# Optimization experiments

Hardware: AMD Instinct MI355X
Metric: run time of the kernel (lower is better)

Reference implementation:

```python
import jax, jax.numpy as jnp
import numpy as np

D_IN, E, K = 128, 256, 16
LN_EPS = 1e-5


def _layernorm(h, g, b):
    mu = jnp.mean(h, axis=-1, keepdims=True)
    var = jnp.mean(jnp.square(h - mu), axis=-1, keepdims=True)
    return (h - mu) * jax.lax.rsqrt(var + LN_EPS) * g + b


def _gelu(h):
    return jax.nn.gelu(h, approximate=False)  # torch F.gelu default = exact erf


def setup_inputs() -> dict:
    key = jax.random.key(0)
    ks = jax.random.split(key, 8)
    B, N = 8, 2048
    def lin(k, fan_in, fan_out):
        bound = 1.0 / np.sqrt(fan_in)
        return jax.random.uniform(k, (fan_in, fan_out), jnp.float32, -bound, bound)
    return {
        "x": jax.random.normal(ks[0], (B, N, D_IN), jnp.float32),
        "coordinates": jax.random.normal(ks[1], (B, N, 3), jnp.float32),
        "W1": lin(ks[2], 2 * D_IN, E), "b1": jnp.zeros((E,), jnp.float32),
        "g1": jnp.ones((E,), jnp.float32), "be1": jnp.zeros((E,), jnp.float32),
        "W2": lin(ks[3], E, E), "b2": jnp.zeros((E,), jnp.float32),
        "g2": jnp.ones((E,), jnp.float32), "be2": jnp.zeros((E,), jnp.float32),
        "W3": lin(ks[4], E, E), "b3": jnp.zeros((E,), jnp.float32),
        "g3": jnp.ones((E,), jnp.float32), "be3": jnp.zeros((E,), jnp.float32),
        "Ws": lin(ks[5], D_IN, E), "bs": jnp.zeros((E,), jnp.float32),
    }


def reference(x, coordinates, W1, b1, g1, be1, W2, b2, g2, be2, W3, b3, g3, be3, Ws, bs):
    B, N, D = x.shape
    # --- dynamic kNN graph: squared euclidean distances (sqrt is monotone, skip it) ---
    sq = jnp.sum(coordinates * coordinates, axis=-1)                 # [B,N]
    d2 = sq[:, :, None] + sq[:, None, :] - 2.0 * jnp.einsum(
        'bnc,bmc->bnm', coordinates, coordinates)                    # [B,N,N]
    d2 = jnp.maximum(d2, 0.0)
    _, idx = jax.lax.top_k(-d2, K)                                   # [B,N,K] nearest (incl. self)
    # --- gather neighbor features: neighbors[b,n,j] = x[b, idx[b,n,j]] ---
    neighbors = jax.vmap(lambda xb, ib: xb[ib])(x, idx)              # [B,N,K,D]
    central = jnp.broadcast_to(x[:, :, None, :], (B, N, K, D))       # [B,N,K,D]
    edge = jnp.concatenate([central, neighbors - central], axis=-1)  # [B,N,K,2D]
    # --- edge MLP: (Linear -> LN -> GELU) x3 ---
    h = _gelu(_layernorm(edge @ W1 + b1, g1, be1))
    h = _gelu(_layernorm(h @ W2 + b2, g2, be2))
    h = _gelu(_layernorm(h @ W3 + b3, g3, be3))                      # [B,N,K,E]
    # --- max aggregate over neighbors + shortcut ---
    agg = jnp.max(h, axis=2)                                         # [B,N,E]
    return _gelu(agg + x @ Ws + bs)
```

## Files before the change

### kernel.cpp

```cpp
#include <hip/hip_runtime.h>
#include <hip/hip_bf16.h>
#include <math.h>

#define B_ 8
#define N_ 2048
#define D_ 128
#define E_ 256
#define K_ 16
#define LN_EPS 1e-5f

typedef short bf16x8 __attribute__((ext_vector_type(8)));
typedef float f32x4 __attribute__((ext_vector_type(4)));
typedef float f32x2 __attribute__((ext_vector_type(2)));

__device__ __forceinline__ float sq3_ref(float x, float y, float z) {
#pragma clang fp contract(off)
    float s = x * x + y * y;
    s = s + z * z;
    return s;
}
__device__ __forceinline__ float d2_ref(float qx, float qy, float qz, float sqq,
                                        float mx, float my, float mz, float sqm) {
#pragma clang fp contract(off)
    float dot = mx * qx + my * qy;
    dot = dot + mz * qz;
    float t1 = sqq + sqm;
    float t2 = 2.0f * dot;
    float d2 = t1 - t2;
    return d2 > 0.0f ? d2 : 0.0f;
}

__device__ __forceinline__ unsigned pack2(float a, float b) {
    union { __hip_bfloat162 h2; unsigned u; } cv;
    cv.h2 = __float22bfloat162_rn(float2{a, b});
    return cv.u;
}

__device__ __forceinline__ f32x2 gelu2(f32x2 v) {
    const f32x2 w = v * v;
    f32x2 inner = w * 0.044715f;
    inner.x += 1.0f; inner.y += 1.0f;
    const f32x2 ue = (v * -2.3022083f) * inner;
    f32x2 t;
    t.x = __builtin_amdgcn_exp2f(ue.x);
    t.y = __builtin_amdgcn_exp2f(ue.y);
    f32x2 den = t;
    den.x += 1.0f; den.y += 1.0f;
    f32x2 r;
    r.x = __builtin_amdgcn_rcpf(den.x);
    r.y = __builtin_amdgcn_rcpf(den.y);
    return v * r;
}

__device__ __forceinline__ float dpp_rowmax16(float v) {
    int x = __float_as_int(v);
    v = fmaxf(v, __int_as_float(__builtin_amdgcn_mov_dpp(x, 0xB1, 0xF, 0xF, true)));
    x = __float_as_int(v);
    v = fmaxf(v, __int_as_float(__builtin_amdgcn_mov_dpp(x, 0x4E, 0xF, 0xF, true)));
    x = __float_as_int(v);
    v = fmaxf(v, __int_as_float(__builtin_amdgcn_mov_dpp(x, 0x141, 0xF, 0xF, true)));
    x = __float_as_int(v);
    v = fmaxf(v, __int_as_float(__builtin_amdgcn_mov_dpp(x, 0x140, 0xF, 0xF, true)));
    return v;
}

__global__ __launch_bounds__(512) void knn_select_kernel(const float* __restrict__ coords,
                                                         int* __restrict__ knn_out) {
    __shared__ float lc[3][N_];
    __shared__ float lsq[N_];
    __shared__ int cnt[8];
    const int wave = threadIdx.x >> 6;
    const int lane = threadIdx.x & 63;
    const int p = blockIdx.x * 8 + wave;
    const int b = p >> 11;
    const int n0 = p & (N_ - 1);
    const float* cb = coords + (size_t)b * N_ * 3;
    for (int i = threadIdx.x; i < N_ * 3; i += 512) {
        int n = i / 3, c = i - 3 * n;
        lc[c][n] = cb[i];
    }
    __syncthreads();
    for (int n = threadIdx.x; n < N_; n += 512) lsq[n] = sq3_ref(lc[0][n], lc[1][n], lc[2][n]);
    __syncthreads();

    const float qx = lc[0][n0], qy = lc[1][n0], qz = lc[2][n0], sqq = lsq[n0];
    unsigned key[32];
#pragma unroll
    for (int j = 0; j < 32; ++j) {
        const int m = j * 64 + lane;
        key[j] = __float_as_uint(d2_ref(qx, qy, qz, sqq, lc[0][m], lc[1][m], lc[2][m], lsq[m]));
    }

    unsigned prefix = 0;
    int rem = K_, setc = N_, bshift = 0;
    bool bounded = false;
    for (int bit = 31; bit >= 0; --bit) {
        const unsigned want = prefix << 1;
        int c = 0;
#pragma unroll
        for (int j = 0; j < 32; ++j) c += ((key[j] >> bit) == want) ? 1 : 0;
        for (int off = 1; off < 64; off <<= 1) c += __shfl_xor(c, off, 64);
        if (rem <= c) { prefix = want; setc = c; }
        else          { prefix = want | 1u; rem -= c; setc -= c; }
        bshift = bit;
        if (setc == rem) { bounded = true; break; }
    }

    if (lane == 0) cnt[wave] = 0;
    int* op = knn_out + (size_t)p * K_;
    const unsigned long long BE = bounded ? (((unsigned long long)prefix + 1ull) << bshift)
                                          : (unsigned long long)prefix;
#pragma unroll
    for (int j = 0; j < 32; ++j) {
        if ((unsigned long long)key[j] < BE) {
            int s = atomicAdd(&cnt[wave], 1);
            op[s] = j * 64 + lane;
        }
    }
    if (!bounded) {
        const unsigned V = prefix;
#pragma unroll
        for (int j = 0; j < 32; ++j) {
            if (rem > 0) {
                unsigned long long mask = __ballot(key[j] == V);
                int below = __popcll(mask & ((1ull << lane) - 1ull));
                if (key[j] == V && below < rem) {
                    int s = atomicAdd(&cnt[wave], 1);
                    op[s] = j * 64 + lane;
                }
                rem -= __popcll(mask);
            }
        }
    }
}

__global__ __launch_bounds__(64) void wprep_kernel(const float* __restrict__ W1,
                                                   const float* __restrict__ W2,
                                                   const float* __restrict__ W3,
                                                   const float* __restrict__ Ws,
                                                   short* __restrict__ WF) {
    const int bi = blockIdx.x;
    const int lane = threadIdx.x;
    const int g = lane >> 4, e = lane & 15;
    const float* W;
    int mt, kt;
    if (bi < 384) {
        const int L = bi >> 7;
        const int t = bi & 127;
        kt = t >> 4; mt = t & 15;
        W = (L == 0) ? W1 : (L == 1) ? W2 : W3;
    } else {
        const int t = bi - 384;
        kt = t >> 4; mt = t & 15;
        W = Ws;
    }
    const int f = 16 * mt + e;
    unsigned v[4];
#pragma unroll
    for (int i2 = 0; i2 < 4; ++i2) {
        const int k = 32 * kt + 8 * g + 2 * i2;
        v[i2] = pack2(W[(size_t)k * E_ + f], W[(size_t)(k + 1) * E_ + f]);
    }
    uint4 u; u.x = v[0]; u.y = v[1]; u.z = v[2]; u.w = v[3];
    *reinterpret_cast<uint4*>(WF + ((size_t)bi * 64 + lane) * 8) = u;
}

#define WCHUNKS 28

__device__ __forceinline__ void stage_chunk(const short* __restrict__ WF,
                                            short* __restrict__ dst,
                                            int c, int wave, int lane) {
    const short* src = WF + ((size_t)(c << 4) << 9);
#pragma unroll
    for (int i = 0; i < 4; ++i) {
        const int slot = (i << 8) + (wave << 6);
        const short* gp = src + ((size_t)(slot + lane) << 3);
        short* lp = dst + ((size_t)slot << 3);
        __builtin_amdgcn_global_load_lds(
            (const __attribute__((address_space(1))) void*)gp,
            (__attribute__((address_space(3))) void*)lp, 16, 0, 0);
    }
}

__global__ __launch_bounds__(256, 2) void edgeconv_mfma(
    const float* __restrict__ x, const int* __restrict__ knn,
    const short* __restrict__ WF,
    const float* __restrict__ b1, const float* __restrict__ g1, const float* __restrict__ be1,
    const float* __restrict__ b2, const float* __restrict__ g2, const float* __restrict__ be2,
    const float* __restrict__ b3, const float* __restrict__ g3, const float* __restrict__ be3,
    const float* __restrict__ bs,
    float* __restrict__ out)
{
    __shared__ short Hl[2][2][4096];
    __shared__ short Wbuf[2][8192];
    __shared__ short Hx[2][2][128];
    __shared__ float4 Xch[2][2][16];
    __shared__ float Pl[9 * 256];
    const int tid  = threadIdx.x;
    const int wave = tid >> 6;
    const int lane = tid & 63;
    const int wq = wave & 1;
    const int pr = wave >> 1;
    const int e = lane & 15;
    const int g = lane >> 4;
    const int p = blockIdx.x * 4 + wave;
    const int b = p >> 11;
    const int n = p & (N_ - 1);
    const unsigned swz = (unsigned)((e & 7) << 4);
    char* Hown = (char*)&Hl[pr][wq][0];
    char* Hp0  = (char*)&Hl[pr][0][0];
    char* Hp1  = (char*)&Hl[pr][1][0];
    char* XCo  = (char*)&Hx[pr][wq][0];
    const char* XC0 = (const char*)&Hx[pr][0][0];
    const char* XC1 = (const char*)&Hx[pr][1][0];

    stage_chunk(WF, &Wbuf[0][0], 0, wave, lane);

    {
        const float* srcs[9] = {b1, g1, be1, b2, g2, be2, b3, g3, be3};
#pragma unroll
        for (int a = 0; a < 9; ++a) Pl[a * 256 + tid] = srcs[a][tid];
    }

    {
        const float4* xr = (const float4*)(x + ((size_t)b * N_ + n) * D_);
        const int nb = knn[(size_t)p * K_ + e];
        const float4* nr = (const float4*)(x + ((size_t)b * N_ + nb) * D_);
#pragma unroll
        for (int c2 = 0; c2 < 8; ++c2) {
            const float4 cv = xr[8 * g + c2];
            const float4 nv = nr[8 * g + c2];
            const int base = (e << 9) + (g << 6) + (c2 << 3);
            const uint2 cpk = make_uint2(pack2(cv.x, cv.y), pack2(cv.z, cv.w));
            *(uint2*)(Hown + (base ^ swz)) = cpk;
            *(uint2*)(Hown + ((base + 256) ^ swz)) =
                make_uint2(pack2(nv.x - cv.x, nv.y - cv.y), pack2(nv.z - cv.z, nv.w - cv.w));
            if (e == 0) *(uint2*)(XCo + (g << 6) + (c2 << 3)) = cpk;
        }
    }

    f32x4 acc0[8], acc1[8];
    int pb = 0;
    const f32x4 z4 = {0.f, 0.f, 0.f, 0.f};

    for (int L = 0; L < 3; ++L) {
        const float* PlL = &Pl[L * 768];
#pragma unroll
        for (int mtl = 0; mtl < 8; ++mtl) { acc0[mtl] = z4; acc1[mtl] = z4; }

        for (int kt = 0; kt < 8; ++kt) {
            const int c = L * 8 + kt;
            asm volatile("s_waitcnt vmcnt(0)" ::: "memory");
            __syncthreads();
            if (c + 1 < WCHUNKS) stage_chunk(WF, &Wbuf[pb ^ 1][0], c + 1, wave, lane);
            const int offB = (int)((unsigned)((e << 9) + (kt << 6) + (g << 4)) ^ swz);
            const bf16x8 Bc0 = *(const bf16x8*)(Hp0 + offB);
            const bf16x8 Bc1 = *(const bf16x8*)(Hp1 + offB);
            const short* Wc = &Wbuf[pb][0];
            __builtin_amdgcn_s_setprio(1);
#pragma unroll
            for (int mtl = 0; mtl < 8; ++mtl) {
                const bf16x8 a = *(const bf16x8*)(Wc + ((((wq << 3) + mtl) << 6) + lane) * 8);
                acc0[mtl] = __builtin_amdgcn_mfma_f32_16x16x32_bf16(a, Bc0, acc0[mtl], 0, 0, 0);
                acc1[mtl] = __builtin_amdgcn_mfma_f32_16x16x32_bf16(a, Bc1, acc1[mtl], 0, 0, 0);
            }
            __builtin_amdgcn_s_setprio(0);
            pb ^= 1;
        }

        f32x2 s2_0 = {0.f, 0.f}, q2_0 = {0.f, 0.f};
        f32x2 s2_1 = {0.f, 0.f}, q2_1 = {0.f, 0.f};
#pragma unroll
        for (int mtl = 0; mtl < 8; ++mtl) {
            const int mtg = (wq << 3) + mtl;
            const float4 bv = *(const float4*)(PlL + mtg * 16 + (g << 2));
            const f32x2 blo = {bv.x, bv.y}, bhi = {bv.z, bv.w};
            f32x2 a0lo = {acc0[mtl][0], acc0[mtl][1]};
            f32x2 a0hi = {acc0[mtl][2], acc0[mtl][3]};
            f32x2 a1lo = {acc1[mtl][0], acc1[mtl][1]};
            f32x2 a1hi = {acc1[mtl][2], acc1[mtl][3]};
            a0lo = a0lo + blo; a0hi = a0hi + bhi;
            a1lo = a1lo + blo; a1hi = a1hi + bhi;
            s2_0 = s2_0 + a0lo; s2_0 = s2_0 + a0hi;
            q2_0 = q2_0 + a0lo * a0lo; q2_0 = q2_0 + a0hi * a0hi;
            s2_1 = s2_1 + a1lo; s2_1 = s2_1 + a1hi;
            q2_1 = q2_1 + a1lo * a1lo; q2_1 = q2_1 + a1hi * a1hi;
            acc0[mtl][0] = a0lo.x; acc0[mtl][1] = a0lo.y;
            acc0[mtl][2] = a0hi.x; acc0[mtl][3] = a0hi.y;
            acc1[mtl][0] = a1lo.x; acc1[mtl][1] = a1lo.y;
            acc1[mtl][2] = a1hi.x; acc1[mtl][3] = a1hi.y;
        }
        float s0 = s2_0.x + s2_0.y, q0 = q2_0.x + q2_0.y;
        float s1 = s2_1.x + s2_1.y, q1 = q2_1.x + q2_1.y;
        s0 += __shfl_xor(s0, 16, 64); s0 += __shfl_xor(s0, 32, 64);
        q0 += __shfl_xor(q0, 16, 64); q0 += __shfl_xor(q0, 32, 64);
        s1 += __shfl_xor(s1, 16, 64); s1 += __shfl_xor(s1, 32, 64);
        q1 += __shfl_xor(q1, 16, 64); q1 += __shfl_xor(q1, 32, 64);
        if (lane < 16) Xch[pr][wq][e] = make_float4(s0, q0, s1, q1);
        __syncthreads();
        const float4 oX = Xch[pr][wq ^ 1][e];
        const float mu0 = (s0 + oX.x) * (1.0f / 256.0f);
        const float var0 = fmaf(-mu0, mu0, (q0 + oX.y) * (1.0f / 256.0f));
        const float rstd0 = rsqrtf(var0 + LN_EPS);
        const float mu1 = (s1 + oX.z) * (1.0f / 256.0f);
        const float var1 = fmaf(-mu1, mu1, (q1 + oX.w) * (1.0f / 256.0f));
        const float rstd1 = rsqrtf(var1 + LN_EPS);

#pragma unroll
        for (int mtl = 0; mtl < 8; ++mtl) {
            const int mtg = (wq << 3) + mtl;
            const float4 gv  = *(const float4*)(PlL + 256 + mtg * 16 + (g << 2));
            const float4 bev = *(const float4*)(PlL + 512 + mtg * 16 + (g << 2));
            const f32x2 glo = {gv.x, gv.y}, ghi = {gv.z, gv.w};
            const f32x2 belo = {bev.x, bev.y}, behi = {bev.z, bev.w};
            const f32x2 A0lo = glo * rstd0, A0hi = ghi * rstd0;
            const f32x2 C0lo = A0lo * (-mu0) + belo, C0hi = A0hi * (-mu0) + behi;
            const f32x2 v0lo = {acc0[mtl][0], acc0[mtl][1]};
            const f32x2 v0hi = {acc0[mtl][2], acc0[mtl][3]};
            const f32x2 r0lo = gelu2(v0lo * A0lo + C0lo);
            const f32x2 r0hi = gelu2(v0hi * A0hi + C0hi);
            const f32x2 A1lo = glo * rstd1, A1hi = ghi * rstd1;
            const f32x2 C1lo = A1lo * (-mu1) + belo, C1hi = A1hi * (-mu1) + behi;
            const f32x2 v1lo = {acc1[mtl][0], acc1[mtl][1]};
            const f32x2 v1hi = {acc1[mtl][2], acc1[mtl][3]};
            const f32x2 r1lo = gelu2(v1lo * A1lo + C1lo);
            const f32x2 r1hi = gelu2(v1hi * A1hi + C1hi);
            if (L < 2) {
                const int wb = (int)((unsigned)((e << 9) + (mtg << 5) + (g << 3)) ^ swz);
                *(uint2*)(Hp0 + wb) = make_uint2(pack2(r0lo.x, r0lo.y), pack2(r0hi.x, r0hi.y));
                *(uint2*)(Hp1 + wb) = make_uint2(pack2(r1lo.x, r1lo.y), pack2(r1hi.x, r1hi.y));
            } else {
                acc0[mtl][0] = r0lo.x; acc0[mtl][1] = r0lo.y;
                acc0[mtl][2] = r0hi.x; acc0[mtl][3] = r0hi.y;
                acc1[mtl][0] = r1lo.x; acc1[mtl][1] = r1lo.y;
                acc1[mtl][2] = r1hi.x; acc1[mtl][3] = r1hi.y;
            }
        }
    }

#pragma unroll
    for (int mtl = 0; mtl < 8; ++mtl) {
#pragma unroll
        for (int i = 0; i < 4; ++i) {
            acc0[mtl][i] = dpp_rowmax16(acc0[mtl][i]);
            acc1[mtl][i] = dpp_rowmax16(acc1[mtl][i]);
        }
    }
    float* Sb0 = (float*)Hp0;
    float* Sb1 = (float*)Hp1;
#pragma unroll
    for (int mtl = 0; mtl < 8; ++mtl) {
        if (e == mtl) {
            const int fo = (((wq << 3) + mtl) << 4) + (g << 2);
            *(float4*)(Sb0 + fo) = *(const float4*)&acc0[mtl];
            *(float4*)(Sb1 + fo) = *(const float4*)&acc1[mtl];
        }
    }

#pragma unroll
    for (int mtl = 0; mtl < 8; ++mtl) { acc0[mtl] = z4; acc1[mtl] = z4; }
    for (int kt = 0; kt < 4; ++kt) {
        const int c = 24 + kt;
        asm volatile("s_waitcnt vmcnt(0)" ::: "memory");
        __syncthreads();
        if (c + 1 < WCHUNKS) stage_chunk(WF, &Wbuf[pb ^ 1][0], c + 1, wave, lane);
        const bf16x8 bx0 = *(const bf16x8*)(XC0 + (kt << 6) + (g << 4));
        const bf16x8 bx1 = *(const bf16x8*)(XC1 + (kt << 6) + (g << 4));
        const short* Wc = &Wbuf[pb][0];
        __builtin_amdgcn_s_setprio(1);
#pragma unroll
        for (int mtl = 0; mtl < 8; ++mtl) {
            const bf16x8 a = *(const bf16x8*)(Wc + ((((wq << 3) + mtl) << 6) + lane) * 8);
            acc0[mtl] = __builtin_amdgcn_mfma_f32_16x16x32_bf16(a, bx0, acc0[mtl], 0, 0, 0);
            acc1[mtl] = __builtin_amdgcn_mfma_f32_16x16x32_bf16(a, bx1, acc1[mtl], 0, 0, 0);
        }
        __builtin_amdgcn_s_setprio(0);
        pb ^= 1;
    }
#pragma unroll
    for (int mtl = 0; mtl < 8; ++mtl) {
        if (e == mtl) {
            const int fo = (((wq << 3) + mtl) << 4) + (g << 2);
            *(float4*)(Sb0 + 256 + fo) = *(const float4*)&acc0[mtl];
            *(float4*)(Sb1 + 256 + fo) = *(const float4*)&acc1[mtl];
        }
    }
    __syncthreads();

    const int f0 = 16 * e + (g << 2);
    const float* SbO = wq ? Sb1 : Sb0;
    const float4 agg = *(const float4*)(SbO + f0);
    const float4 ssc = *(const float4*)(SbO + 256 + f0);
    const float4 bsv = *(const float4*)(bs + f0);
    f32x2 elo = {agg.x + ssc.x, agg.y + ssc.y};
    f32x2 ehi = {agg.z + ssc.z, agg.w + ssc.w};
    const f32x2 blo = {bsv.x, bsv.y}, bhi = {bsv.z, bsv.w};
    const f32x2 olo = gelu2(elo + blo);
    const f32x2 ohi = gelu2(ehi + bhi);
    float4 o;
    o.x = olo.x; o.y = olo.y; o.z = ohi.x; o.w = ohi.y;
    *(float4*)(out + (size_t)p * E_ + f0) = o;
}

extern "C" void kernel_launch(void* const* d_in, const int* in_sizes, int n_in,
                              void* d_out, int out_size, void* d_ws, size_t ws_size,
                              hipStream_t stream) {
    const float* x      = (const float*)d_in[0];
    const float* coords = (const float*)d_in[1];
    const float* W1  = (const float*)d_in[2];
    const float* b1  = (const float*)d_in[3];
    const float* g1  = (const float*)d_in[4];
    const float* be1 = (const float*)d_in[5];
    const float* W2  = (const float*)d_in[6];
    const float* b2  = (const float*)d_in[7];
    const float* g2  = (const float*)d_in[8];
    const float* be2 = (const float*)d_in[9];
    const float* W3  = (const float*)d_in[10];
    const float* b3  = (const float*)d_in[11];
    const float* g3  = (const float*)d_in[12];
    const float* be3 = (const float*)d_in[13];
    const float* Ws  = (const float*)d_in[14];
    const float* bs  = (const float*)d_in[15];
    float* out = (float*)d_out;

    int*   knn = (int*)d_ws;
    short* WF  = (short*)((char*)d_ws + (1 << 20));

    wprep_kernel<<<448, 64, 0, stream>>>(W1, W2, W3, Ws, WF);
    knn_select_kernel<<<B_ * (N_ / 8), 512, 0, stream>>>(coords, knn);
    edgeconv_mfma<<<(B_ * N_) / 4, 256, 0, stream>>>(
        x, knn, WF, b1, g1, be1, b2, g2, be2, b3, g3, be3, bs, out);
}
```

Baseline: 333.6 us.

## Move shortcut projection x@Ws into a separate MFMA kernel with full tile reuse

The shortcut GEMM x@Ws+bs is taken out of the edge-conv kernel and computed by a new kernel in which each wave handles 16 points at full MFMA width. Its result is written to the output buffer, and the edge-conv kernel later reads it back before applying the final GELU. Before, the shortcut ran inside edgeconv with only 2 points per block pair, so each MFMA tile was mostly wasted and 4 extra weight-chunk stages and barriers were needed. In exchange the change adds a kernel launch and an extra global write and read of the output.

```diff
diff --git a/kernel.cpp b/kernel.cpp
--- a/kernel.cpp
+++ b/kernel.cpp
@@ -165,7 +165,47 @@
     *reinterpret_cast<uint4*>(WF + ((size_t)bi * 64 + lane) * 8) = u;
 }
 
-#define WCHUNKS 28
+__global__ __launch_bounds__(256) void shortcut_kernel(const float* __restrict__ x,
+                                                       const short* __restrict__ WF,
+                                                       const float* __restrict__ bs,
+                                                       float* __restrict__ out) {
+    const int wave = threadIdx.x >> 6;
+    const int lane = threadIdx.x & 63;
+    const int e = lane & 15;
+    const int g = lane >> 4;
+    const int p0 = (blockIdx.x * 4 + wave) * 16;
+    const float* xr = x + (size_t)(p0 + e) * D_;
+    const short* WSF = WF + (size_t)(24 * 16) * 512;
+
+    f32x4 acc[16];
+    const f32x4 z4 = {0.f, 0.f, 0.f, 0.f};
+#pragma unroll
+    for (int mt = 0; mt < 16; ++mt) acc[mt] = z4;
+
+#pragma unroll
+    for (int kt = 0; kt < 4; ++kt) {
+        const float4 xa = *(const float4*)(xr + kt * 32 + g * 8);
+        const float4 xb = *(const float4*)(xr + kt * 32 + g * 8 + 4);
+        union { unsigned u[4]; bf16x8 v; } bx;
+        bx.u[0] = pack2(xa.x, xa.y); bx.u[1] = pack2(xa.z, xa.w);
+        bx.u[2] = pack2(xb.x, xb.y); bx.u[3] = pack2(xb.z, xb.w);
+#pragma unroll
+        for (int mt = 0; mt < 16; ++mt) {
+            const bf16x8 a = *(const bf16x8*)(WSF + ((size_t)(kt * 16 + mt) * 64 + lane) * 8);
+            acc[mt] = __builtin_amdgcn_mfma_f32_16x16x32_bf16(a, bx.v, acc[mt], 0, 0, 0);
+        }
+    }
+#pragma unroll
+    for (int mt = 0; mt < 16; ++mt) {
+        const float4 bsv = *(const float4*)(bs + 16 * mt + 4 * g);
+        float4 o;
+        o.x = acc[mt][0] + bsv.x; o.y = acc[mt][1] + bsv.y;
+        o.z = acc[mt][2] + bsv.z; o.w = acc[mt][3] + bsv.w;
+        *(float4*)(out + (size_t)(p0 + e) * E_ + 16 * mt + 4 * g) = o;
+    }
+}
+
+#define WCHUNKS 24
 
 __device__ __forceinline__ void stage_chunk(const short* __restrict__ WF,
                                             short* __restrict__ dst,
@@ -188,12 +228,10 @@
     const float* __restrict__ b1, const float* __restrict__ g1, const float* __restrict__ be1,
     const float* __restrict__ b2, const float* __restrict__ g2, const float* __restrict__ be2,
     const float* __restrict__ b3, const float* __restrict__ g3, const float* __restrict__ be3,
-    const float* __restrict__ bs,
     float* __restrict__ out)
 {
     __shared__ short Hl[2][2][4096];
     __shared__ short Wbuf[2][8192];
-    __shared__ short Hx[2][2][128];
     __shared__ float4 Xch[2][2][16];
     __shared__ float Pl[9 * 256];
     const int tid  = threadIdx.x;
@@ -210,9 +248,6 @@
     char* Hown = (char*)&Hl[pr][wq][0];
     char* Hp0  = (char*)&Hl[pr][0][0];
     char* Hp1  = (char*)&Hl[pr][1][0];
-    char* XCo  = (char*)&Hx[pr][wq][0];
-    const char* XC0 = (const char*)&Hx[pr][0][0];
-    const char* XC1 = (const char*)&Hx[pr][1][0];
 
     stage_chunk(WF, &Wbuf[0][0], 0, wave, lane);
 
@@ -231,11 +266,9 @@
             const float4 cv = xr[8 * g + c2];
             const float4 nv = nr[8 * g + c2];
             const int base = (e << 9) + (g << 6) + (c2 << 3);
-            const uint2 cpk = make_uint2(pack2(cv.x, cv.y), pack2(cv.z, cv.w));
-            *(uint2*)(Hown + (base ^ swz)) = cpk;
+            *(uint2*)(Hown + (base ^ swz)) = make_uint2(pack2(cv.x, cv.y), pack2(cv.z, cv.w));
             *(uint2*)(Hown + ((base + 256) ^ swz)) =
                 make_uint2(pack2(nv.x - cv.x, nv.y - cv.y), pack2(nv.z - cv.z, nv.w - cv.w));
-            if (e == 0) *(uint2*)(XCo + (g << 6) + (c2 << 3)) = cpk;
         }
     }
 
@@ -356,50 +389,20 @@
             *(float4*)(Sb1 + fo) = *(const float4*)&acc1[mtl];
         }
     }
-
-#pragma unroll
-    for (int mtl = 0; mtl < 8; ++mtl) { acc0[mtl] = z4; acc1[mtl] = z4; }
-    for (int kt = 0; kt < 4; ++kt) {
-        const int c = 24 + kt;
-        asm volatile("s_waitcnt vmcnt(0)" ::: "memory");
-        __syncthreads();
-        if (c + 1 < WCHUNKS) stage_chunk(WF, &Wbuf[pb ^ 1][0], c + 1, wave, lane);
-        const bf16x8 bx0 = *(const bf16x8*)(XC0 + (kt << 6) + (g << 4));
-        const bf16x8 bx1 = *(const bf16x8*)(XC1 + (kt << 6) + (g << 4));
-        const short* Wc = &Wbuf[pb][0];
-        __builtin_amdgcn_s_setprio(1);
-#pragma unroll
-        for (int mtl = 0; mtl < 8; ++mtl) {
-            const bf16x8 a = *(const bf16x8*)(Wc + ((((wq << 3) + mtl) << 6) + lane) * 8);
-            acc0[mtl] = __builtin_amdgcn_mfma_f32_16x16x32_bf16(a, bx0, acc0[mtl], 0, 0, 0);
-            acc1[mtl] = __builtin_amdgcn_mfma_f32_16x16x32_bf16(a, bx1, acc1[mtl], 0, 0, 0);
-        }
-        __builtin_amdgcn_s_setprio(0);
-        pb ^= 1;
-    }
-#pragma unroll
-    for (int mtl = 0; mtl < 8; ++mtl) {
-        if (e == mtl) {
-            const int fo = (((wq << 3) + mtl) << 4) + (g << 2);
-            *(float4*)(Sb0 + 256 + fo) = *(const float4*)&acc0[mtl];
-            *(float4*)(Sb1 + 256 + fo) = *(const float4*)&acc1[mtl];
-        }
-    }
     __syncthreads();
 
     const int f0 = 16 * e + (g << 2);
     const float* SbO = wq ? Sb1 : Sb0;
     const float4 agg = *(const float4*)(SbO + f0);
-    const float4 ssc = *(const float4*)(SbO + 256 + f0);
-    const float4 bsv = *(const float4*)(bs + f0);
+    float* op = out + (size_t)p * E_ + f0;
+    const float4 ssc = *(const float4*)op;
     f32x2 elo = {agg.x + ssc.x, agg.y + ssc.y};
     f32x2 ehi = {agg.z + ssc.z, agg.w + ssc.w};
-    const f32x2 blo = {bsv.x, bsv.y}, bhi = {bsv.z, bsv.w};
-    const f32x2 olo = gelu2(elo + blo);
-    const f32x2 ohi = gelu2(ehi + bhi);
+    const f32x2 olo = gelu2(elo);
+    const f32x2 ohi = gelu2(ehi);
     float4 o;
     o.x = olo.x; o.y = olo.y; o.z = ohi.x; o.w = ohi.y;
-    *(float4*)(out + (size_t)p * E_ + f0) = o;
+    *(float4*)op = o;
 }
 
 extern "C" void kernel_launch(void* const* d_in, const int* in_sizes, int n_in,
@@ -428,6 +431,7 @@
 
     wprep_kernel<<<448, 64, 0, stream>>>(W1, W2, W3, Ws, WF);
     knn_select_kernel<<<B_ * (N_ / 8), 512, 0, stream>>>(coords, knn);
+    shortcut_kernel<<<(B_ * N_) / 64, 256, 0, stream>>>(x, WF, bs, out);
     edgeconv_mfma<<<(B_ * N_) / 4, 256, 0, stream>>>(
-        x, knn, WF, b1, g1, be1, b2, g2, be2, b3, g3, be3, bs, out);
-}
+        x, knn, WF, b1, g1, be1, b2, g2, be2, b3, g3, be3, out);
+}
```

Result: no change. 330.2 us (-1.0%).
